# Kernel optimization log

Hardware: AMD Instinct MI355X
Metric: run time of the kernel (lower is better)

Reference implementation:

```python
import jax, jax.numpy as jnp
import numpy as np

N_GRAPHS = 1024
N_NODES = 65536
N_EDGES = 262144
D = 256          # node/edge/global feature dim
D_IN = 3 * D     # concat of edge_agg, node_agg, globals
D_HID = 512
D_OUT = 256


def setup_inputs() -> dict:
    key = jax.random.key(0)
    ks = jax.random.split(key, 9)
    nodes = jax.random.normal(ks[0], (N_NODES, D), dtype=jnp.float32)
    edges = jax.random.normal(ks[1], (N_EDGES, D), dtype=jnp.float32)
    globals_ = jax.random.normal(ks[2], (N_GRAPHS, D), dtype=jnp.float32)
    node_graph_ids = jnp.sort(jax.random.randint(ks[3], (N_NODES,), 0, N_GRAPHS, dtype=jnp.int32))
    edge_graph_ids = jnp.sort(jax.random.randint(ks[4], (N_EDGES,), 0, N_GRAPHS, dtype=jnp.int32))
    W1 = jax.random.normal(ks[5], (D_IN, D_HID), dtype=jnp.float32) * (1.0 / np.sqrt(D_IN))
    b1 = jnp.zeros((D_HID,), dtype=jnp.float32)
    W2 = jax.random.normal(ks[6], (D_HID, D_OUT), dtype=jnp.float32) * (1.0 / np.sqrt(D_HID))
    b2 = jnp.zeros((D_OUT,), dtype=jnp.float32)
    return {"nodes": nodes, "edges": edges, "globals_": globals_,
            "node_graph_ids": node_graph_ids, "edge_graph_ids": edge_graph_ids,
            "W1": W1, "b1": b1, "W2": W2, "b2": b2}


def reference(nodes, edges, globals_, node_graph_ids, edge_graph_ids, W1, b1, W2, b2):
    G = globals_.shape[0]
    # EdgesToGlobalsAggregator / NodesToGlobalsAggregator: unsorted segment sum per graph
    edge_agg = jax.ops.segment_sum(edges, edge_graph_ids, num_segments=G)  # [G, D]
    node_agg = jax.ops.segment_sum(nodes, node_graph_ids, num_segments=G)  # [G, D]
    collected = jnp.concatenate([edge_agg, node_agg, globals_], axis=-1)   # [G, 3D]
    # global_model: 2-layer MLP with ReLU
    h = jax.nn.relu(collected @ W1 + b1)
    updated_globals = h @ W2 + b2
    return updated_globals
```

## Files before the change

kernel.cpp:

```cpp
#include <hip/hip_runtime.h>

#define G      1024
#define NNODES 65536
#define NEDGES 262144
#define D      256
#define DIN    768
#define DHID   512
#define DOUT   256

__device__ __forceinline__ int lower_bound(const int* __restrict__ a, int n, int key) {
    int lo = 0, hi = n;
    while (lo < hi) {
        const int mid = (lo + hi) >> 1;
        if (a[mid] < key) lo = mid + 1; else hi = mid;
    }
    return lo;
}

__global__ __launch_bounds__(256) void fused_agg(
        const float4* __restrict__ nodes,
        const float4* __restrict__ edges,
        const float4* __restrict__ globals_,
        const int* __restrict__ nids,
        const int* __restrict__ eids,
        float* __restrict__ collected) {
    const int g    = blockIdx.x;
    const int lane = threadIdx.x & 63;
    const int wave = threadIdx.x >> 6;

    const int es = lower_bound(eids, NEDGES, g);
    const int ee = lower_bound(eids, NEDGES, g + 1);
    const int ns = lower_bound(nids, NNODES, g);
    const int ne = lower_bound(nids, NNODES, g + 1);

    float4 acc_e = {0.f, 0.f, 0.f, 0.f};
    {
        int r = es + wave;
        for (; r + 12 < ee; r += 16) {
            const float4 v0 = edges[(size_t)(r +  0) * (D / 4) + lane];
            const float4 v1 = edges[(size_t)(r +  4) * (D / 4) + lane];
            const float4 v2 = edges[(size_t)(r +  8) * (D / 4) + lane];
            const float4 v3 = edges[(size_t)(r + 12) * (D / 4) + lane];
            acc_e.x += (v0.x + v1.x) + (v2.x + v3.x);
            acc_e.y += (v0.y + v1.y) + (v2.y + v3.y);
            acc_e.z += (v0.z + v1.z) + (v2.z + v3.z);
            acc_e.w += (v0.w + v1.w) + (v2.w + v3.w);
        }
        for (; r < ee; r += 4) {
            const float4 v = edges[(size_t)r * (D / 4) + lane];
            acc_e.x += v.x; acc_e.y += v.y; acc_e.z += v.z; acc_e.w += v.w;
        }
    }

    float4 acc_n = {0.f, 0.f, 0.f, 0.f};
    {
        int r = ns + wave;
        for (; r + 12 < ne; r += 16) {
            const float4 v0 = nodes[(size_t)(r +  0) * (D / 4) + lane];
            const float4 v1 = nodes[(size_t)(r +  4) * (D / 4) + lane];
            const float4 v2 = nodes[(size_t)(r +  8) * (D / 4) + lane];
            const float4 v3 = nodes[(size_t)(r + 12) * (D / 4) + lane];
            acc_n.x += (v0.x + v1.x) + (v2.x + v3.x);
            acc_n.y += (v0.y + v1.y) + (v2.y + v3.y);
            acc_n.z += (v0.z + v1.z) + (v2.z + v3.z);
            acc_n.w += (v0.w + v1.w) + (v2.w + v3.w);
        }
        for (; r < ne; r += 4) {
            const float4 v = nodes[(size_t)r * (D / 4) + lane];
            acc_n.x += v.x; acc_n.y += v.y; acc_n.z += v.z; acc_n.w += v.w;
        }
    }

    __shared__ __align__(16) float se[4][D];
    __shared__ __align__(16) float sn[4][D];
    *(float4*)&se[wave][lane * 4] = acc_e;
    *(float4*)&sn[wave][lane * 4] = acc_n;
    __syncthreads();

    const int t = threadIdx.x;
    const float ev = (se[0][t] + se[1][t]) + (se[2][t] + se[3][t]);
    const float nv = (sn[0][t] + sn[1][t]) + (sn[2][t] + sn[3][t]);
    float* row = collected + (size_t)g * DIN;
    row[t]           = ev;
    row[D + t]       = nv;
    row[2 * D + t]   = ((const float*)globals_)[(size_t)g * D + t];
}

template <int TM, int TN, int TK>
__global__ __launch_bounds__(256) void gemm_bias_act(
        const float* __restrict__ A, const float* __restrict__ B,
        const float* __restrict__ bias, float* __restrict__ C,
        int M, int N, int K, int relu) {
    __shared__ float As[TM][TK + 1];
    __shared__ __align__(16) float Bs[TK][TN];

    const int tid = threadIdx.x;
    const int tx = tid & 15;
    const int ty = tid >> 4;
    const int m0 = blockIdx.y * TM;
    const int n0 = blockIdx.x * TN;

    float4 acc0 = {0.f, 0.f, 0.f, 0.f};
    float4 acc1 = {0.f, 0.f, 0.f, 0.f};

    for (int kt = 0; kt < K; kt += TK) {
        {
            const int r = tid >> 3;
            const int c = (tid & 7) * 4;
            const float4 a4 = *(const float4*)&A[(size_t)(m0 + r) * K + kt + c];
            As[r][c] = a4.x; As[r][c + 1] = a4.y; As[r][c + 2] = a4.z; As[r][c + 3] = a4.w;
        }
        {
            const int r = tid >> 3;
            const int c = (tid & 7) * 8;
            *(float4*)&Bs[r][c]     = *(const float4*)&B[(size_t)(kt + r) * N + n0 + c];
            *(float4*)&Bs[r][c + 4] = *(const float4*)&B[(size_t)(kt + r) * N + n0 + c + 4];
        }
        __syncthreads();
#pragma unroll
        for (int k = 0; k < TK; ++k) {
            const float a0 = As[ty * 2 + 0][k];
            const float a1 = As[ty * 2 + 1][k];
            const float4 bv = *(const float4*)&Bs[k][tx * 4];
            acc0.x += a0 * bv.x; acc0.y += a0 * bv.y;
            acc0.z += a0 * bv.z; acc0.w += a0 * bv.w;
            acc1.x += a1 * bv.x; acc1.y += a1 * bv.y;
            acc1.z += a1 * bv.z; acc1.w += a1 * bv.w;
        }
        __syncthreads();
    }

    const int col = n0 + tx * 4;
    const int row = m0 + ty * 2;
    const float4 bv = *(const float4*)&bias[col];
    float4 o0, o1;
    o0.x = acc0.x + bv.x; o0.y = acc0.y + bv.y; o0.z = acc0.z + bv.z; o0.w = acc0.w + bv.w;
    o1.x = acc1.x + bv.x; o1.y = acc1.y + bv.y; o1.z = acc1.z + bv.z; o1.w = acc1.w + bv.w;
    if (relu) {
        o0.x = fmaxf(o0.x, 0.f); o0.y = fmaxf(o0.y, 0.f);
        o0.z = fmaxf(o0.z, 0.f); o0.w = fmaxf(o0.w, 0.f);
        o1.x = fmaxf(o1.x, 0.f); o1.y = fmaxf(o1.y, 0.f);
        o1.z = fmaxf(o1.z, 0.f); o1.w = fmaxf(o1.w, 0.f);
    }
    *(float4*)&C[(size_t)row * N + col] = o0;
    *(float4*)&C[(size_t)(row + 1) * N + col] = o1;
}

extern "C" void kernel_launch(void* const* d_in, const int* in_sizes, int n_in,
                              void* d_out, int out_size, void* d_ws, size_t ws_size,
                              hipStream_t stream) {
    const float* nodes    = (const float*)d_in[0];
    const float* edges    = (const float*)d_in[1];
    const float* globals_ = (const float*)d_in[2];
    const int*   nids     = (const int*)d_in[3];
    const int*   eids     = (const int*)d_in[4];
    const float* W1       = (const float*)d_in[5];
    const float* b1       = (const float*)d_in[6];
    const float* W2       = (const float*)d_in[7];
    const float* b2       = (const float*)d_in[8];
    float* out = (float*)d_out;

    float* collected = (float*)d_ws;
    float* h         = collected + (size_t)G * DIN;

    fused_agg<<<G, 256, 0, stream>>>(
        (const float4*)nodes, (const float4*)edges, (const float4*)globals_,
        nids, eids, collected);

    gemm_bias_act<32, 64, 32><<<dim3(DHID / 64, G / 32), 256, 0, stream>>>(
        collected, W1, b1, h, G, DHID, DIN, 1);

    gemm_bias_act<32, 64, 32><<<dim3(DOUT / 64, G / 32), 256, 0, stream>>>(
        h, W2, b2, out, G, DOUT, DHID, 0);
}
```

Before: 477.7 us.

## Double-buffer GEMM shared tiles and deepen segment-sum unrolling

The GEMM kernel now double-buffers its shared-memory tiles, prefetching the next K-tile into registers while the current tile is computed, and cuts synchronisation to one barrier per iteration. A is stored transposed so each thread reads its two A values with a single float2 load. The aggregation loops unroll to 8 outstanding row loads per wave instead of 4, to raise memory-level parallelism in the bandwidth-bound reduction. This costs more registers and double the shared memory per block, which may lower occupancy.

```diff
diff --git a/kernel.cpp b/kernel.cpp
--- a/kernel.cpp
+++ b/kernel.cpp
@@ -36,15 +36,19 @@
     float4 acc_e = {0.f, 0.f, 0.f, 0.f};
     {
         int r = es + wave;
-        for (; r + 12 < ee; r += 16) {
+        for (; r + 28 < ee; r += 32) {
             const float4 v0 = edges[(size_t)(r +  0) * (D / 4) + lane];
             const float4 v1 = edges[(size_t)(r +  4) * (D / 4) + lane];
             const float4 v2 = edges[(size_t)(r +  8) * (D / 4) + lane];
             const float4 v3 = edges[(size_t)(r + 12) * (D / 4) + lane];
-            acc_e.x += (v0.x + v1.x) + (v2.x + v3.x);
-            acc_e.y += (v0.y + v1.y) + (v2.y + v3.y);
-            acc_e.z += (v0.z + v1.z) + (v2.z + v3.z);
-            acc_e.w += (v0.w + v1.w) + (v2.w + v3.w);
+            const float4 v4 = edges[(size_t)(r + 16) * (D / 4) + lane];
+            const float4 v5 = edges[(size_t)(r + 20) * (D / 4) + lane];
+            const float4 v6 = edges[(size_t)(r + 24) * (D / 4) + lane];
+            const float4 v7 = edges[(size_t)(r + 28) * (D / 4) + lane];
+            acc_e.x += ((v0.x + v1.x) + (v2.x + v3.x)) + ((v4.x + v5.x) + (v6.x + v7.x));
+            acc_e.y += ((v0.y + v1.y) + (v2.y + v3.y)) + ((v4.y + v5.y) + (v6.y + v7.y));
+            acc_e.z += ((v0.z + v1.z) + (v2.z + v3.z)) + ((v4.z + v5.z) + (v6.z + v7.z));
+            acc_e.w += ((v0.w + v1.w) + (v2.w + v3.w)) + ((v4.w + v5.w) + (v6.w + v7.w));
         }
         for (; r < ee; r += 4) {
             const float4 v = edges[(size_t)r * (D / 4) + lane];
@@ -55,15 +59,19 @@
     float4 acc_n = {0.f, 0.f, 0.f, 0.f};
     {
         int r = ns + wave;
-        for (; r + 12 < ne; r += 16) {
+        for (; r + 28 < ne; r += 32) {
             const float4 v0 = nodes[(size_t)(r +  0) * (D / 4) + lane];
             const float4 v1 = nodes[(size_t)(r +  4) * (D / 4) + lane];
             const float4 v2 = nodes[(size_t)(r +  8) * (D / 4) + lane];
             const float4 v3 = nodes[(size_t)(r + 12) * (D / 4) + lane];
-            acc_n.x += (v0.x + v1.x) + (v2.x + v3.x);
-            acc_n.y += (v0.y + v1.y) + (v2.y + v3.y);
-            acc_n.z += (v0.z + v1.z) + (v2.z + v3.z);
-            acc_n.w += (v0.w + v1.w) + (v2.w + v3.w);
+            const float4 v4 = nodes[(size_t)(r + 16) * (D / 4) + lane];
+            const float4 v5 = nodes[(size_t)(r + 20) * (D / 4) + lane];
+            const float4 v6 = nodes[(size_t)(r + 24) * (D / 4) + lane];
+            const float4 v7 = nodes[(size_t)(r + 28) * (D / 4) + lane];
+            acc_n.x += ((v0.x + v1.x) + (v2.x + v3.x)) + ((v4.x + v5.x) + (v6.x + v7.x));
+            acc_n.y += ((v0.y + v1.y) + (v2.y + v3.y)) + ((v4.y + v5.y) + (v6.y + v7.y));
+            acc_n.z += ((v0.z + v1.z) + (v2.z + v3.z)) + ((v4.z + v5.z) + (v6.z + v7.z));
+            acc_n.w += ((v0.w + v1.w) + (v2.w + v3.w)) + ((v4.w + v5.w) + (v6.w + v7.w));
         }
         for (; r < ne; r += 4) {
             const float4 v = nodes[(size_t)r * (D / 4) + lane];
@@ -81,9 +89,9 @@
     const float ev = (se[0][t] + se[1][t]) + (se[2][t] + se[3][t]);
     const float nv = (sn[0][t] + sn[1][t]) + (sn[2][t] + sn[3][t]);
     float* row = collected + (size_t)g * DIN;
-    row[t]           = ev;
-    row[D + t]       = nv;
-    row[2 * D + t]   = ((const float*)globals_)[(size_t)g * D + t];
+    row[t]         = ev;
+    row[D + t]     = nv;
+    row[2 * D + t] = ((const float*)globals_)[(size_t)g * D + t];
 }
 
 template <int TM, int TN, int TK>
@@ -91,8 +99,8 @@
         const float* __restrict__ A, const float* __restrict__ B,
         const float* __restrict__ bias, float* __restrict__ C,
         int M, int N, int K, int relu) {
-    __shared__ float As[TM][TK + 1];
-    __shared__ __align__(16) float Bs[TK][TN];
+    __shared__ float At[2][TK][TM + 2];
+    __shared__ __align__(16) float Bs[2][TK][TN];
 
     const int tid = threadIdx.x;
     const int tx = tid & 15;
@@ -100,34 +108,55 @@
     const int m0 = blockIdx.y * TM;
     const int n0 = blockIdx.x * TN;
 
+    const int ar = tid >> 3;
+    const int ac = (tid & 7) * 4;
+    const int br = tid >> 3;
+    const int bc = (tid & 7) * 8;
+
+    const float* Aptr = A + (size_t)(m0 + ar) * K + ac;
+    const float* Bptr = B + (size_t)br * N + n0 + bc;
+
+    {
+        const float4 a4  = *(const float4*)Aptr;
+        const float4 b40 = *(const float4*)Bptr;
+        const float4 b41 = *(const float4*)(Bptr + 4);
+        At[0][ac + 0][ar] = a4.x; At[0][ac + 1][ar] = a4.y;
+        At[0][ac + 2][ar] = a4.z; At[0][ac + 3][ar] = a4.w;
+        *(float4*)&Bs[0][br][bc]     = b40;
+        *(float4*)&Bs[0][br][bc + 4] = b41;
+    }
+    __syncthreads();
+
     float4 acc0 = {0.f, 0.f, 0.f, 0.f};
     float4 acc1 = {0.f, 0.f, 0.f, 0.f};
+    int buf = 0;
 
     for (int kt = 0; kt < K; kt += TK) {
-        {
-            const int r = tid >> 3;
-            const int c = (tid & 7) * 4;
-            const float4 a4 = *(const float4*)&A[(size_t)(m0 + r) * K + kt + c];
-            As[r][c] = a4.x; As[r][c + 1] = a4.y; As[r][c + 2] = a4.z; As[r][c + 3] = a4.w;
-        }
-        {
-            const int r = tid >> 3;
-            const int c = (tid & 7) * 8;
-            *(float4*)&Bs[r][c]     = *(const float4*)&B[(size_t)(kt + r) * N + n0 + c];
-            *(float4*)&Bs[r][c + 4] = *(const float4*)&B[(size_t)(kt + r) * N + n0 + c + 4];
-        }
-        __syncthreads();
+        const bool has_next = (kt + TK) < K;
+        float4 na, nb0, nb1;
+        if (has_next) {
+            na  = *(const float4*)(Aptr + kt + TK);
+            nb0 = *(const float4*)(Bptr + (size_t)(kt + TK) * N);
+            nb1 = *(const float4*)(Bptr + (size_t)(kt + TK) * N + 4);
+        }
 #pragma unroll
         for (int k = 0; k < TK; ++k) {
-            const float a0 = As[ty * 2 + 0][k];
-            const float a1 = As[ty * 2 + 1][k];
-            const float4 bv = *(const float4*)&Bs[k][tx * 4];
-            acc0.x += a0 * bv.x; acc0.y += a0 * bv.y;
-            acc0.z += a0 * bv.z; acc0.w += a0 * bv.w;
-            acc1.x += a1 * bv.x; acc1.y += a1 * bv.y;
-            acc1.z += a1 * bv.z; acc1.w += a1 * bv.w;
-        }
-        __syncthreads();
+            const float2 a2 = *(const float2*)&At[buf][k][ty * 2];
+            const float4 bv = *(const float4*)&Bs[buf][k][tx * 4];
+            acc0.x += a2.x * bv.x; acc0.y += a2.x * bv.y;
+            acc0.z += a2.x * bv.z; acc0.w += a2.x * bv.w;
+            acc1.x += a2.y * bv.x; acc1.y += a2.y * bv.y;
+            acc1.z += a2.y * bv.z; acc1.w += a2.y * bv.w;
+        }
+        if (has_next) {
+            const int nb = buf ^ 1;
+            At[nb][ac + 0][ar] = na.x; At[nb][ac + 1][ar] = na.y;
+            At[nb][ac + 2][ar] = na.z; At[nb][ac + 3][ar] = na.w;
+            *(float4*)&Bs[nb][br][bc]     = nb0;
+            *(float4*)&Bs[nb][br][bc + 4] = nb1;
+            __syncthreads();
+            buf = nb;
+        }
     }
 
     const int col = n0 + tx * 4;
```

New measurement: 465.2 us. 2.6% less time.
